# Kernel tuning notes

Hardware: AMD Instinct MI355X
Metric: run time of the kernel (lower is better)

The kernel has to match this reference:

```python
import jax, jax.numpy as jnp
import numpy as np

N = 50000
E = 800000
IN_DIM = 128
F_NUM = 64
OUT_DIM = 16


def gcn_norm(edge_index, edge_weight, num_nodes):
    # add self loops with fill value 1.0 (improved=False), then symmetric norm
    e = edge_index.shape[1]
    w = jnp.ones((e,), jnp.float32) if edge_weight is None else edge_weight
    loop = jnp.arange(num_nodes, dtype=edge_index.dtype)
    row = jnp.concatenate([edge_index[0], loop])
    col = jnp.concatenate([edge_index[1], loop])
    w = jnp.concatenate([w, jnp.ones((num_nodes,), jnp.float32)])
    deg = jax.ops.segment_sum(w, col, num_segments=num_nodes)
    dis = jnp.where(deg > 0, jax.lax.rsqrt(jnp.where(deg > 0, deg, 1.0)), 0.0)
    norm = dis[row] * w * dis[col]
    return row, col, norm


def dgconv(x, edge_index, edge_weight, num_nodes):
    row, col, norm = gcn_norm(edge_index, edge_weight, num_nodes)
    # gather -> scale -> scatter-add
    msg = norm[:, None] * x[row]          # [E+N, F]
    return jax.ops.segment_sum(msg, col, num_segments=num_nodes)


def setup_inputs() -> dict:
    key = jax.random.key(0)
    ks = jax.random.split(key, 12)
    x = jax.random.normal(ks[0], (N, IN_DIM), jnp.float32)
    edge_index = jax.random.randint(ks[1], (2, E), 0, N, jnp.int64 if jax.config.jax_enable_x64 else jnp.int32)
    edge_in = jax.random.randint(ks[2], (2, E), 0, N, edge_index.dtype)
    edge_out = jax.random.randint(ks[3], (2, E), 0, N, edge_index.dtype)
    in_w = jax.random.uniform(ks[4], (E,), jnp.float32)
    out_w = jax.random.uniform(ks[5], (E,), jnp.float32)
    lin1_w = jax.random.normal(ks[6], (F_NUM, IN_DIM), jnp.float32) / np.sqrt(IN_DIM)
    lin2_w = jax.random.normal(ks[7], (F_NUM, 3 * F_NUM), jnp.float32) / np.sqrt(3 * F_NUM)
    bias1 = jnp.zeros((1, F_NUM), jnp.float32)
    bias2 = jnp.zeros((1, F_NUM), jnp.float32)
    conv_w = jax.random.normal(ks[8], (OUT_DIM, 3 * F_NUM), jnp.float32) / np.sqrt(3 * F_NUM)
    conv_b = jnp.zeros((OUT_DIM,), jnp.float32)
    return {"x": x, "edge_index": edge_index, "edge_in": edge_in, "edge_out": edge_out,
            "in_w": in_w, "out_w": out_w, "lin1_w": lin1_w, "lin2_w": lin2_w,
            "bias1": bias1, "bias2": bias2, "conv_w": conv_w, "conv_b": conv_b}


def reference(x, edge_index, edge_in, edge_out, in_w, out_w,
              lin1_w, lin2_w, bias1, bias2, conv_w, conv_b):
    n = x.shape[0]
    h = x @ lin1_w.T                                          # [N, F]
    h1 = dgconv(h, edge_index, None, n) + bias1
    h2 = dgconv(h, edge_in, in_w, n) + bias1
    h3 = dgconv(h, edge_out, out_w, n) + bias1
    h = jax.nn.relu(jnp.concatenate([h1, h2, h3], axis=-1))   # [N, 3F]
    h = h @ lin2_w.T                                          # [N, F]
    h1 = dgconv(h, edge_index, None, n) + bias2
    h2 = dgconv(h, edge_in, in_w, n) + bias2
    h3 = dgconv(h, edge_out, out_w, n) + bias2
    h = jax.nn.relu(jnp.concatenate([h1, h2, h3], axis=-1))   # [N, 3F]
    # Conv1d(kernel_size=1) == pointwise linear over channels
    logits = h @ conv_w.T + conv_b                            # [N, out_dim]
    return jax.nn.log_softmax(logits, axis=1)
```

## Files before the change

kernel.cpp:

```cpp
#include <hip/hip_runtime.h>
#include <hip/hip_fp16.h>
#include <math.h>

#define FDIM 64
#define CATDIM 192
#define CH 2048
#define MAXNB 1024
#define SCTILE 2048


__global__ __launch_bounds__(256) void k_chist(const int* __restrict__ ei0,
                                               const int* __restrict__ ei1,
                                               const int* __restrict__ ei2,
                                               int* __restrict__ bhT,
                                               int NB, int nchunks, int E) {
    __shared__ int hist[MAXNB];
    const int c = blockIdx.x, g = blockIdx.y, tid = threadIdx.x;
    const int* dest = (g == 0 ? ei0 : g == 1 ? ei1 : ei2) + E;
    const size_t L = (size_t)NB * nchunks;

    for (int i = tid; i < NB; i += 256) hist[i] = 0;
    __syncthreads();

    const int lo = c * CH, hi = min(E, lo + CH);
    for (int i = lo + tid; i < hi; i += 256) atomicAdd(&hist[dest[i] >> 6], 1);
    __syncthreads();

    for (int i = tid; i < NB; i += 256)
        bhT[g * L + (size_t)c * NB + i] = hist[i];
}


__global__ __launch_bounds__(256) void k_tr(const int* __restrict__ in,
                                            int* __restrict__ out,
                                            int rows, int cols) {
    __shared__ int tile[32][33];
    const int g = blockIdx.z;
    const int c0 = blockIdx.x * 32;
    const int r0 = blockIdx.y * 32;
    const int tx = threadIdx.x & 31, ty0 = threadIdx.x >> 5;
    const size_t L = (size_t)rows * cols;
    const int* pin = in + (size_t)g * L;
    int* pout = out + (size_t)g * L;

    for (int dy = 0; dy < 32; dy += 8) {
        int r = r0 + ty0 + dy, c = c0 + tx;
        tile[ty0 + dy][tx] = (r < rows && c < cols) ? pin[(size_t)r * cols + c] : 0;
    }
    __syncthreads();
    for (int dy = 0; dy < 32; dy += 8) {
        int c = c0 + ty0 + dy, r = r0 + tx;
        if (c < cols && r < rows) pout[(size_t)c * rows + r] = tile[tx][ty0 + dy];
    }
}


__global__ __launch_bounds__(256) void k_scan_a(const int* __restrict__ bh,
                                                int* __restrict__ bsum,
                                                int L, int nblkS) {
    __shared__ int s[256];
    const int b = blockIdx.x, g = blockIdx.y, tid = threadIdx.x;
    const int* data = bh + (size_t)g * L;
    const int base = b * SCTILE + tid * 8;
    int v = 0;
#pragma unroll
    for (int j = 0; j < 8; ++j) {
        int idx = base + j;
        if (idx < L) v += data[idx];
    }
    s[tid] = v;
    __syncthreads();
    for (int d = 128; d > 0; d >>= 1) {
        if (tid < d) s[tid] += s[tid + d];
        __syncthreads();
    }
    if (tid == 0) bsum[g * nblkS + b] = s[0];
}

__global__ __launch_bounds__(256) void k_scan_b(int* __restrict__ bsum, int nblkS) {
    __shared__ int s[256];
    const int g = blockIdx.x, tid = threadIdx.x;
    int v = (tid < nblkS) ? bsum[g * nblkS + tid] : 0;
    s[tid] = v;
    __syncthreads();
    for (int d = 1; d < 256; d <<= 1) {
        int t = (tid >= d) ? s[tid - d] : 0;
        __syncthreads();
        s[tid] += t;
        __syncthreads();
    }
    if (tid < nblkS) bsum[g * nblkS + tid] = s[tid] - v;
}

__global__ __launch_bounds__(256) void k_scan_c(int* __restrict__ bh,
                                                const int* __restrict__ bsum,
                                                int L, int nblkS) {
    __shared__ int s[256];
    const int b = blockIdx.x, g = blockIdx.y, tid = threadIdx.x;
    int* data = bh + (size_t)g * L;
    const int base = b * SCTILE + tid * 8;

    int e[8];
    int tot = 0;
#pragma unroll
    for (int j = 0; j < 8; ++j) {
        e[j] = (base + j < L) ? data[base + j] : 0;
        tot += e[j];
    }
    s[tid] = tot;
    __syncthreads();
    for (int d = 1; d < 256; d <<= 1) {
        int t = (tid >= d) ? s[tid - d] : 0;
        __syncthreads();
        s[tid] += t;
        __syncthreads();
    }
    int run = bsum[g * nblkS + b] + s[tid] - tot;
#pragma unroll
    for (int j = 0; j < 8; ++j) {
        if (base + j < L) {
            int v = e[j];
            data[base + j] = run;
            run += v;
        }
    }
}


__global__ void k_bbase(const int* __restrict__ bh, int* __restrict__ bbase,
                        int NB, int nchunks, int E) {
    int i = blockIdx.x * blockDim.x + threadIdx.x;
    if (i >= 3 * NB) return;
    int g = i / NB, b = i - g * NB;
    bbase[g * (NB + 1) + b] = bh[((size_t)g * NB + b) * nchunks];
    if (b == 0) bbase[g * (NB + 1) + NB] = E;
}


__global__ __launch_bounds__(256) void k_cfill(const int* __restrict__ ei0,
                                               const int* __restrict__ ei1,
                                               const int* __restrict__ ei2,
                                               const float* __restrict__ w1,
                                               const float* __restrict__ w2,
                                               const int* __restrict__ bhT2,
                                               int2* __restrict__ barr,
                                               int NB, int nchunks, int E) {
    __shared__ int cur[MAXNB];
    const int c = blockIdx.x, g = blockIdx.y, tid = threadIdx.x;
    const int* e = (g == 0 ? ei0 : g == 1 ? ei1 : ei2);
    const float* w = (g == 1 ? w1 : w2);
    const int* srcp = e;
    const int* dest = e + E;
    int2* bout = barr + (size_t)g * E;
    const size_t L = (size_t)NB * nchunks;

    for (int i = tid; i < NB; i += 256)
        cur[i] = bhT2[g * L + (size_t)c * NB + i];
    __syncthreads();

    const int lo = c * CH, hi = min(E, lo + CH);
    for (int i = lo + tid; i < hi; i += 256) {
        int d = dest[i];
        int slot = atomicAdd(&cur[d >> 6], 1);
        float wv = (g == 0) ? 0.f : w[i];
        bout[slot] = make_int2(srcp[i] | ((d & 63) << 16), __float_as_int(wv));
    }
}


__global__ __launch_bounds__(256) void k_deg(const int2* __restrict__ barr,
                                             const int* __restrict__ bbase,
                                             int* __restrict__ rowptr,
                                             float* __restrict__ dis,
                                             int N, int E, int NB) {
    __shared__ int hist[64];
    __shared__ float wsum[64];
    __shared__ int sc[64];

    const int b = blockIdx.x, g = blockIdx.y, tid = threadIdx.x;
    const int2* bin = barr + (size_t)g * E;
    const int beg = bbase[g * (NB + 1) + b];
    const int end = bbase[g * (NB + 1) + b + 1];

    if (tid < 64) { hist[tid] = 0; wsum[tid] = 1.0f; }
    __syncthreads();

    for (int t = beg + tid; t < end; t += 256) {
        int2 p = bin[t];
        int dl = (p.x >> 16) & 63;
        atomicAdd(&hist[dl], 1);
        if (g) atomicAdd(&wsum[dl], __int_as_float(p.y));
    }
    __syncthreads();

    if (tid < 64) sc[tid] = hist[tid];
    __syncthreads();
    for (int d = 1; d < 64; d <<= 1) {
        int t = 0;
        if (tid < 64 && tid >= d) t = sc[tid - d];
        __syncthreads();
        if (tid < 64) sc[tid] += t;
        __syncthreads();
    }
    if (tid < 64) {
        int node = b * 64 + tid;
        if (node < N) {
            rowptr[g * (N + 1) + node] = beg + (sc[tid] - hist[tid]);
            float s = g ? wsum[tid] : (1.0f + (float)hist[tid]);
            dis[g * N + node] = rsqrtf(s);
        }
    }
    if (b == NB - 1 && tid == 0) rowptr[g * (N + 1) + N] = end;
}


__global__ __launch_bounds__(256) void k_place(const int2* __restrict__ barr,
                                               const int* __restrict__ bbase,
                                               const int* __restrict__ rowptr,
                                               const float* __restrict__ dis,
                                               unsigned* __restrict__ csr,
                                               int N, int E, int NB) {
    __shared__ int cur[64];
    const int b = blockIdx.x, g = blockIdx.y, tid = threadIdx.x;
    const int2* bin = barr + (size_t)g * E;
    const int beg = bbase[g * (NB + 1) + b];
    const int end = bbase[g * (NB + 1) + b + 1];

    if (tid < 64) {
        int node = b * 64 + tid;
        cur[tid] = (node < N) ? rowptr[g * (N + 1) + node] - beg : 0;
    }
    __syncthreads();

    for (int t = beg + tid; t < end; t += 256) {
        int2 p = bin[t];
        int dl = (p.x >> 16) & 63;
        int pos = atomicAdd(&cur[dl], 1);
        int src = p.x & 0xFFFF;
        float wv = g ? __int_as_float(p.y) : 1.0f;
        float v = wv * dis[g * N + src];
        unsigned short wb = __half_as_ushort(__float2half(v));
        csr[(size_t)g * E + beg + pos] = (unsigned)src | ((unsigned)wb << 16);
    }
}


template <typename T> __device__ inline float4 load4f(const T* p);
template <> __device__ inline float4 load4f<float>(const float* p) {
    return *reinterpret_cast<const float4*>(p);
}
template <> __device__ inline float4 load4f<__half>(const __half* p) {
    __half2 a = *reinterpret_cast<const __half2*>(p);
    __half2 b = *reinterpret_cast<const __half2*>(p + 2);
    float2 fa = __half22float2(a), fb = __half22float2(b);
    return make_float4(fa.x, fa.y, fb.x, fb.y);
}

template <int K, typename TA>
__global__ __launch_bounds__(256) void k_gemm(const TA* __restrict__ A,
                                              const float* __restrict__ W,
                                              __half* __restrict__ out, int n) {
    __shared__ float wt[K * 65];
    __shared__ float xs[64 * 36];

    const int tid = threadIdx.x;
    const int n0 = blockIdx.x * 64;

    for (int idx = tid; idx < FDIM * K; idx += 256) {
        int fr = idx / K;
        int kr = idx - fr * K;
        wt[kr * 65 + fr] = W[idx];
    }

    const int f = tid & 63;
    const int q = tid >> 6;
    float acc[16];
#pragma unroll
    for (int j = 0; j < 16; ++j) acc[j] = 0.f;

    for (int kc = 0; kc < K; kc += 32) {
        __syncthreads();
#pragma unroll
        for (int u = tid; u < 512; u += 256) {
            int node = u >> 3;
            int k4 = u & 7;
            int gn = n0 + node;
            float4 a = make_float4(0.f, 0.f, 0.f, 0.f);
            if (gn < n) a = load4f(&A[(size_t)gn * K + kc + k4 * 4]);
            *reinterpret_cast<float4*>(&xs[node * 36 + k4 * 4]) = a;
        }
        __syncthreads();

#pragma unroll
        for (int kk = 0; kk < 32; kk += 4) {
            float w0 = wt[(kc + kk + 0) * 65 + f];
            float w1 = wt[(kc + kk + 1) * 65 + f];
            float w2 = wt[(kc + kk + 2) * 65 + f];
            float w3 = wt[(kc + kk + 3) * 65 + f];
#pragma unroll
            for (int jj = 0; jj < 16; ++jj) {
                int j = jj * 4 + q;
                float4 av = *reinterpret_cast<const float4*>(&xs[j * 36 + kk]);
                acc[jj] = fmaf(av.x, w0, fmaf(av.y, w1, fmaf(av.z, w2, fmaf(av.w, w3, acc[jj]))));
            }
        }
    }

#pragma unroll
    for (int jj = 0; jj < 16; ++jj) {
        int node = n0 + jj * 4 + q;
        if (node < n) out[(size_t)node * FDIM + f] = __float2half(acc[jj]);
    }
}


__global__ __launch_bounds__(256) void k_gather(const __half* __restrict__ h,
                                                const float* __restrict__ dis,
                                                const int* __restrict__ rowptr,
                                                const unsigned* __restrict__ csr,
                                                const float* __restrict__ bias,
                                                __half* __restrict__ cat,
                                                int N, int E) {
    int i = blockIdx.x * 4 + (threadIdx.x >> 6);
    if (i >= N) return;
    const int lane = threadIdx.x & 63;

    const float hv = __half2float(h[(size_t)i * FDIM + lane]);
    const float b = bias[lane];

#pragma unroll
    for (int g = 0; g < 3; ++g) {
        const int* rp = rowptr + g * (N + 1);
        const unsigned* cg = csr + (size_t)g * E;
        const int beg = __builtin_amdgcn_readfirstlane(rp[i]);
        const int end = __builtin_amdgcn_readfirstlane(rp[i + 1]);
        float dg = dis[g * N + i];

        float acc0 = 0.f, acc1 = 0.f, acc2 = 0.f, acc3 = 0.f;
        float acc4 = 0.f, acc5 = 0.f, acc6 = 0.f, acc7 = 0.f;
        int j = beg;
        for (; j + 8 <= end; j += 8) {
            unsigned u0 = cg[j + 0];
            unsigned u1 = cg[j + 1];
            unsigned u2 = cg[j + 2];
            unsigned u3 = cg[j + 3];
            unsigned u4 = cg[j + 4];
            unsigned u5 = cg[j + 5];
            unsigned u6 = cg[j + 6];
            unsigned u7 = cg[j + 7];
            float a0 = __half2float(h[(size_t)(u0 & 0xFFFFu) * FDIM + lane]);
            float a1 = __half2float(h[(size_t)(u1 & 0xFFFFu) * FDIM + lane]);
            float a2 = __half2float(h[(size_t)(u2 & 0xFFFFu) * FDIM + lane]);
            float a3 = __half2float(h[(size_t)(u3 & 0xFFFFu) * FDIM + lane]);
            float a4 = __half2float(h[(size_t)(u4 & 0xFFFFu) * FDIM + lane]);
            float a5 = __half2float(h[(size_t)(u5 & 0xFFFFu) * FDIM + lane]);
            float a6 = __half2float(h[(size_t)(u6 & 0xFFFFu) * FDIM + lane]);
            float a7 = __half2float(h[(size_t)(u7 & 0xFFFFu) * FDIM + lane]);
            acc0 = fmaf(__half2float(__ushort_as_half((unsigned short)(u0 >> 16))), a0, acc0);
            acc1 = fmaf(__half2float(__ushort_as_half((unsigned short)(u1 >> 16))), a1, acc1);
            acc2 = fmaf(__half2float(__ushort_as_half((unsigned short)(u2 >> 16))), a2, acc2);
            acc3 = fmaf(__half2float(__ushort_as_half((unsigned short)(u3 >> 16))), a3, acc3);
            acc4 = fmaf(__half2float(__ushort_as_half((unsigned short)(u4 >> 16))), a4, acc4);
            acc5 = fmaf(__half2float(__ushort_as_half((unsigned short)(u5 >> 16))), a5, acc5);
            acc6 = fmaf(__half2float(__ushort_as_half((unsigned short)(u6 >> 16))), a6, acc6);
            acc7 = fmaf(__half2float(__ushort_as_half((unsigned short)(u7 >> 16))), a7, acc7);
        }
        if (j + 4 <= end) {
            unsigned u0 = cg[j + 0];
            unsigned u1 = cg[j + 1];
            unsigned u2 = cg[j + 2];
            unsigned u3 = cg[j + 3];
            float a0 = __half2float(h[(size_t)(u0 & 0xFFFFu) * FDIM + lane]);
            float a1 = __half2float(h[(size_t)(u1 & 0xFFFFu) * FDIM + lane]);
            float a2 = __half2float(h[(size_t)(u2 & 0xFFFFu) * FDIM + lane]);
            float a3 = __half2float(h[(size_t)(u3 & 0xFFFFu) * FDIM + lane]);
            acc0 = fmaf(__half2float(__ushort_as_half((unsigned short)(u0 >> 16))), a0, acc0);
            acc1 = fmaf(__half2float(__ushort_as_half((unsigned short)(u1 >> 16))), a1, acc1);
            acc2 = fmaf(__half2float(__ushort_as_half((unsigned short)(u2 >> 16))), a2, acc2);
            acc3 = fmaf(__half2float(__ushort_as_half((unsigned short)(u3 >> 16))), a3, acc3);
            j += 4;
        }
        for (; j < end; ++j) {
            unsigned u0 = cg[j];
            float a0 = __half2float(h[(size_t)(u0 & 0xFFFFu) * FDIM + lane]);
            acc0 = fmaf(__half2float(__ushort_as_half((unsigned short)(u0 >> 16))), a0, acc0);
        }
        float outv = dg * (((acc0 + acc1) + (acc2 + acc3)) + ((acc4 + acc5) + (acc6 + acc7)))
                   + dg * dg * hv + b;
        cat[(size_t)i * CATDIM + g * FDIM + lane] = __float2half(outv > 0.f ? outv : 0.f);
    }
}


__global__ __launch_bounds__(256) void k_final(const __half* __restrict__ cat,
                                               const float* __restrict__ convw,
                                               const float* __restrict__ convb,
                                               float* __restrict__ out, int n) {
    __shared__ float wl[16 * 196];
    __shared__ float bl[16];
    const int tid = threadIdx.x;
    for (int t = tid; t < 16 * 192; t += 256) {
        int o = t / 192;
        int k = t - o * 192;
        wl[o * 196 + k] = convw[t];
    }
    if (tid < 16) bl[tid] = convb[tid];
    __syncthreads();

    const int o = tid & 15;
    const int node = blockIdx.x * 16 + (tid >> 4);
    const int nc = node < n ? node : n - 1;

    const float4* xr4 = reinterpret_cast<const float4*>(cat + (size_t)nc * CATDIM);
    const float* wr = &wl[o * 196];
    float acc = bl[o];
#pragma unroll
    for (int k8 = 0; k8 < CATDIM / 8; ++k8) {
        float4 raw = xr4[k8];
        const __half2* hp = reinterpret_cast<const __half2*>(&raw);
        float2 f0 = __half22float2(hp[0]);
        float2 f1 = __half22float2(hp[1]);
        float2 f2 = __half22float2(hp[2]);
        float2 f3 = __half22float2(hp[3]);
        const float* w8 = wr + k8 * 8;
        acc += f0.x * w8[0] + f0.y * w8[1] + f1.x * w8[2] + f1.y * w8[3] +
               f2.x * w8[4] + f2.y * w8[5] + f3.x * w8[6] + f3.y * w8[7];
    }

    float m = acc;
    m = fmaxf(m, __shfl_xor(m, 1));
    m = fmaxf(m, __shfl_xor(m, 2));
    m = fmaxf(m, __shfl_xor(m, 4));
    m = fmaxf(m, __shfl_xor(m, 8));
    float s = __expf(acc - m);
    s += __shfl_xor(s, 1);
    s += __shfl_xor(s, 2);
    s += __shfl_xor(s, 4);
    s += __shfl_xor(s, 8);
    if (node < n) out[(size_t)node * 16 + o] = acc - m - logf(s);
}


extern "C" void kernel_launch(void* const* d_in, const int* in_sizes, int n_in,
                              void* d_out, int out_size, void* d_ws, size_t ws_size,
                              hipStream_t stream) {
    const float* x      = (const float*)d_in[0];
    const int*   ei     = (const int*)d_in[1];
    const int*   e_in   = (const int*)d_in[2];
    const int*   e_out  = (const int*)d_in[3];
    const float* in_w   = (const float*)d_in[4];
    const float* out_w  = (const float*)d_in[5];
    const float* lin1_w = (const float*)d_in[6];
    const float* lin2_w = (const float*)d_in[7];
    const float* bias1  = (const float*)d_in[8];
    const float* bias2  = (const float*)d_in[9];
    const float* conv_w = (const float*)d_in[10];
    const float* conv_b = (const float*)d_in[11];
    float* out = (float*)d_out;

    const int N = in_sizes[0] / 128;
    const int E = in_sizes[1] / 2;
    const int NB = (N + 63) >> 6;
    const int nchunks = (E + CH - 1) / CH;
    const int L = NB * nchunks;
    const int nblkS = (L + SCTILE - 1) / SCTILE;

    float* ws = (float*)d_ws;
    size_t o = 0;
    float* dis    = ws + o;            o += (size_t)3 * N;
    int*   rowptr = (int*)(ws + o);    o += ((size_t)3 * (N + 1) + 1) & ~1ull;
    int*   bbase  = (int*)(ws + o);    o += ((size_t)3 * (NB + 1) + 1) & ~1ull;
    int*   bsum   = (int*)(ws + o);    o += ((size_t)3 * nblkS + 1) & ~1ull;
    int*   bh     = (int*)(ws + o);    o += ((size_t)3 * L + 3) & ~3ull;
    int*   bhT    = (int*)(ws + o);    o += ((size_t)3 * L + 3) & ~3ull;
    __half* h     = (__half*)(ws + o); o += (size_t)N * (FDIM / 2);
    o = (o + 3) & ~3ull;
    unsigned* csr = (unsigned*)(ws + o); o += (size_t)3 * E;
    o = (o + 3) & ~3ull;
    __half* cat   = (__half*)(ws + o); o += (size_t)N * (CATDIM / 2);
    int2*  barr   = (int2*)cat;

    const int B = 256;

    hipLaunchKernelGGL(k_chist, dim3(nchunks, 3), dim3(B), 0, stream, ei, e_in, e_out, bhT, NB, nchunks, E);
    hipLaunchKernelGGL(k_tr, dim3((NB + 31) / 32, (nchunks + 31) / 32, 3), dim3(B), 0, stream,
                       bhT, bh, nchunks, NB);
    hipLaunchKernelGGL(k_scan_a, dim3(nblkS, 3), dim3(B), 0, stream, bh, bsum, L, nblkS);
    hipLaunchKernelGGL(k_scan_b, dim3(3), dim3(B), 0, stream, bsum, nblkS);
    hipLaunchKernelGGL(k_scan_c, dim3(nblkS, 3), dim3(B), 0, stream, bh, bsum, L, nblkS);
    hipLaunchKernelGGL(k_bbase, dim3((3 * NB + B - 1) / B), dim3(B), 0, stream, bh, bbase, NB, nchunks, E);
    hipLaunchKernelGGL(k_tr, dim3((nchunks + 31) / 32, (NB + 31) / 32, 3), dim3(B), 0, stream,
                       bh, bhT, NB, nchunks);
    hipLaunchKernelGGL(k_cfill, dim3(nchunks, 3), dim3(B), 0, stream,
                       ei, e_in, e_out, in_w, out_w, bhT, barr, NB, nchunks, E);
    hipLaunchKernelGGL(k_deg, dim3(NB, 3), dim3(B), 0, stream, barr, bbase, rowptr, dis, N, E, NB);
    hipLaunchKernelGGL(k_place, dim3(NB, 3), dim3(B), 0, stream, barr, bbase, rowptr, dis, csr, N, E, NB);

    hipLaunchKernelGGL((k_gemm<128, float>), dim3((N + 63) / 64), dim3(B), 0, stream, x, lin1_w, h, N);
    hipLaunchKernelGGL(k_gather, dim3((N + 3) / 4), dim3(B), 0, stream,
                       h, dis, rowptr, csr, bias1, cat, N, E);

    hipLaunchKernelGGL((k_gemm<192, __half>), dim3((N + 63) / 64), dim3(B), 0, stream, cat, lin2_w, h, N);
    hipLaunchKernelGGL(k_gather, dim3((N + 3) / 4), dim3(B), 0, stream,
                       h, dis, rowptr, csr, bias2, cat, N, E);

    hipLaunchKernelGGL(k_final, dim3((N + 15) / 16), dim3(B), 0, stream, cat, conv_w, conv_b, out, N);
}
```

Measured before the change: 413.7 us.

## Fuse final conv+log_softmax into gather, half2 gather lanes, chunk GEMM weights, fold bbase

Several changes land together. The final pointwise conv and log_softmax are fused into the second gather kernel, so the layer-two concat buffer is never written or read back. The gather now has each wave split into two halves that each process alternate edges with half2 feature loads, and the halves are combined with a cross-half shuffle. The GEMM stages weights in K-chunks to cut shared memory use and raise occupancy, and the bucket-base kernel is merged into the scan. In exchange, the fused gather loads the conv weights into LDS in every block and gains some branching in the per-edge index loads.

```diff
diff --git a/kernel.cpp b/kernel.cpp
--- a/kernel.cpp
+++ b/kernel.cpp
@@ -92,9 +92,12 @@
     if (tid < nblkS) bsum[g * nblkS + tid] = s[tid] - v;
 }
 
+
 __global__ __launch_bounds__(256) void k_scan_c(int* __restrict__ bh,
                                                 const int* __restrict__ bsum,
-                                                int L, int nblkS) {
+                                                int* __restrict__ bbase,
+                                                int L, int nblkS,
+                                                int NB, int nchunks, int E) {
     __shared__ int s[256];
     const int b = blockIdx.x, g = blockIdx.y, tid = threadIdx.x;
     int* data = bh + (size_t)g * L;
@@ -118,22 +121,15 @@
     int run = bsum[g * nblkS + b] + s[tid] - tot;
 #pragma unroll
     for (int j = 0; j < 8; ++j) {
-        if (base + j < L) {
+        int idx = base + j;
+        if (idx < L) {
             int v = e[j];
-            data[base + j] = run;
+            data[idx] = run;
+            if (idx % nchunks == 0) bbase[g * (NB + 1) + idx / nchunks] = run;
             run += v;
         }
     }
-}
-
-
-__global__ void k_bbase(const int* __restrict__ bh, int* __restrict__ bbase,
-                        int NB, int nchunks, int E) {
-    int i = blockIdx.x * blockDim.x + threadIdx.x;
-    if (i >= 3 * NB) return;
-    int g = i / NB, b = i - g * NB;
-    bbase[g * (NB + 1) + b] = bh[((size_t)g * NB + b) * nchunks];
-    if (b == 0) bbase[g * (NB + 1) + NB] = E;
+    if (b == 0 && tid == 0) bbase[g * (NB + 1) + NB] = E;
 }
 
 
@@ -256,21 +252,15 @@
     return make_float4(fa.x, fa.y, fb.x, fb.y);
 }
 
-template <int K, typename TA>
+template <int K, int KCH, typename TA>
 __global__ __launch_bounds__(256) void k_gemm(const TA* __restrict__ A,
                                               const float* __restrict__ W,
                                               __half* __restrict__ out, int n) {
-    __shared__ float wt[K * 65];
+    __shared__ float wt[KCH * 65];
     __shared__ float xs[64 * 36];
 
     const int tid = threadIdx.x;
     const int n0 = blockIdx.x * 64;
-
-    for (int idx = tid; idx < FDIM * K; idx += 256) {
-        int fr = idx / K;
-        int kr = idx - fr * K;
-        wt[kr * 65 + fr] = W[idx];
-    }
 
     const int f = tid & 63;
     const int q = tid >> 6;
@@ -280,6 +270,13 @@
 
     for (int kc = 0; kc < K; kc += 32) {
         __syncthreads();
+        if ((kc % KCH) == 0) {
+            for (int idx = tid; idx < FDIM * KCH; idx += 256) {
+                int fr = idx / KCH;
+                int kr = idx - fr * KCH;
+                wt[kr * 65 + fr] = W[fr * K + kc + kr];
+            }
+        }
 #pragma unroll
         for (int u = tid; u < 512; u += 256) {
             int node = u >> 3;
@@ -291,12 +288,13 @@
         }
         __syncthreads();
 
+        const int kb = kc % KCH;
 #pragma unroll
         for (int kk = 0; kk < 32; kk += 4) {
-            float w0 = wt[(kc + kk + 0) * 65 + f];
-            float w1 = wt[(kc + kk + 1) * 65 + f];
-            float w2 = wt[(kc + kk + 2) * 65 + f];
-            float w3 = wt[(kc + kk + 3) * 65 + f];
+            float w0 = wt[(kb + kk + 0) * 65 + f];
+            float w1 = wt[(kb + kk + 1) * 65 + f];
+            float w2 = wt[(kb + kk + 2) * 65 + f];
+            float w3 = wt[(kb + kk + 3) * 65 + f];
 #pragma unroll
             for (int jj = 0; jj < 16; ++jj) {
                 int j = jj * 4 + q;
@@ -314,19 +312,45 @@
 }
 
 
+template <int FUSE>
 __global__ __launch_bounds__(256) void k_gather(const __half* __restrict__ h,
                                                 const float* __restrict__ dis,
                                                 const int* __restrict__ rowptr,
                                                 const unsigned* __restrict__ csr,
                                                 const float* __restrict__ bias,
                                                 __half* __restrict__ cat,
+                                                const float* __restrict__ convw,
+                                                const float* __restrict__ convb,
+                                                float* __restrict__ outp,
                                                 int N, int E) {
-    int i = blockIdx.x * 4 + (threadIdx.x >> 6);
+    __shared__ float wl[FUSE ? 16 * 196 : 1];
+    __shared__ float bl[FUSE ? 16 : 1];
+    __shared__ float scratch[FUSE ? 4 : 1][FUSE ? 192 : 1];
+
+    const int tid = threadIdx.x;
+    if (FUSE) {
+        for (int t = tid; t < 16 * 192; t += 256) {
+            int o = t / 192;
+            int k = t - o * 192;
+            wl[o * 196 + k] = convw[t];
+        }
+        if (tid < 16) bl[tid] = convb[tid];
+        __syncthreads();
+    }
+
+    const int wv = tid >> 6;
+    const int lane = tid & 63;
+    const int fp = lane & 31;
+    const int ep = lane >> 5;
+    const int i = blockIdx.x * 4 + wv;
     if (i >= N) return;
-    const int lane = threadIdx.x & 63;
-
-    const float hv = __half2float(h[(size_t)i * FDIM + lane]);
-    const float b = bias[lane];
+
+    const __half2* h2 = reinterpret_cast<const __half2*>(h);
+    float2 hv = __half22float2(h2[(size_t)i * 32 + fp]);
+    const float b0 = bias[2 * fp];
+    const float b1 = bias[2 * fp + 1];
+
+    float res0[3], res1[3];
 
 #pragma unroll
     for (int g = 0; g < 3; ++g) {
@@ -334,110 +358,100 @@
         const unsigned* cg = csr + (size_t)g * E;
         const int beg = __builtin_amdgcn_readfirstlane(rp[i]);
         const int end = __builtin_amdgcn_readfirstlane(rp[i + 1]);
-        float dg = dis[g * N + i];
-
-        float acc0 = 0.f, acc1 = 0.f, acc2 = 0.f, acc3 = 0.f;
-        float acc4 = 0.f, acc5 = 0.f, acc6 = 0.f, acc7 = 0.f;
+        const float dg = dis[g * N + i];
+
+        float ax0 = 0.f, ay0 = 0.f, ax1 = 0.f, ay1 = 0.f;
+        float ax2 = 0.f, ay2 = 0.f, ax3 = 0.f, ay3 = 0.f;
         int j = beg;
         for (; j + 8 <= end; j += 8) {
-            unsigned u0 = cg[j + 0];
-            unsigned u1 = cg[j + 1];
-            unsigned u2 = cg[j + 2];
-            unsigned u3 = cg[j + 3];
-            unsigned u4 = cg[j + 4];
-            unsigned u5 = cg[j + 5];
-            unsigned u6 = cg[j + 6];
-            unsigned u7 = cg[j + 7];
-            float a0 = __half2float(h[(size_t)(u0 & 0xFFFFu) * FDIM + lane]);
-            float a1 = __half2float(h[(size_t)(u1 & 0xFFFFu) * FDIM + lane]);
-            float a2 = __half2float(h[(size_t)(u2 & 0xFFFFu) * FDIM + lane]);
-            float a3 = __half2float(h[(size_t)(u3 & 0xFFFFu) * FDIM + lane]);
-            float a4 = __half2float(h[(size_t)(u4 & 0xFFFFu) * FDIM + lane]);
-            float a5 = __half2float(h[(size_t)(u5 & 0xFFFFu) * FDIM + lane]);
-            float a6 = __half2float(h[(size_t)(u6 & 0xFFFFu) * FDIM + lane]);
-            float a7 = __half2float(h[(size_t)(u7 & 0xFFFFu) * FDIM + lane]);
-            acc0 = fmaf(__half2float(__ushort_as_half((unsigned short)(u0 >> 16))), a0, acc0);
-            acc1 = fmaf(__half2float(__ushort_as_half((unsigned short)(u1 >> 16))), a1, acc1);
-            acc2 = fmaf(__half2float(__ushort_as_half((unsigned short)(u2 >> 16))), a2, acc2);
-            acc3 = fmaf(__half2float(__ushort_as_half((unsigned short)(u3 >> 16))), a3, acc3);
-            acc4 = fmaf(__half2float(__ushort_as_half((unsigned short)(u4 >> 16))), a4, acc4);
-            acc5 = fmaf(__half2float(__ushort_as_half((unsigned short)(u5 >> 16))), a5, acc5);
-            acc6 = fmaf(__half2float(__ushort_as_half((unsigned short)(u6 >> 16))), a6, acc6);
-            acc7 = fmaf(__half2float(__ushort_as_half((unsigned short)(u7 >> 16))), a7, acc7);
+            unsigned u0 = ep ? cg[j + 1] : cg[j + 0];
+            unsigned u1 = ep ? cg[j + 3] : cg[j + 2];
+            unsigned u2 = ep ? cg[j + 5] : cg[j + 4];
+            unsigned u3 = ep ? cg[j + 7] : cg[j + 6];
+            float2 A0 = __half22float2(h2[(size_t)(u0 & 0xFFFFu) * 32 + fp]);
+            float2 A1 = __half22float2(h2[(size_t)(u1 & 0xFFFFu) * 32 + fp]);
+            float2 A2 = __half22float2(h2[(size_t)(u2 & 0xFFFFu) * 32 + fp]);
+            float2 A3 = __half22float2(h2[(size_t)(u3 & 0xFFFFu) * 32 + fp]);
+            float w0 = __half2float(__ushort_as_half((unsigned short)(u0 >> 16)));
+            float w1 = __half2float(__ushort_as_half((unsigned short)(u1 >> 16)));
+            float w2 = __half2float(__ushort_as_half((unsigned short)(u2 >> 16)));
+            float w3 = __half2float(__ushort_as_half((unsigned short)(u3 >> 16)));
+            ax0 = fmaf(w0, A0.x, ax0); ay0 = fmaf(w0, A0.y, ay0);
+            ax1 = fmaf(w1, A1.x, ax1); ay1 = fmaf(w1, A1.y, ay1);
+            ax2 = fmaf(w2, A2.x, ax2); ay2 = fmaf(w2, A2.y, ay2);
+            ax3 = fmaf(w3, A3.x, ax3); ay3 = fmaf(w3, A3.y, ay3);
         }
         if (j + 4 <= end) {
-            unsigned u0 = cg[j + 0];
-            unsigned u1 = cg[j + 1];
-            unsigned u2 = cg[j + 2];
-            unsigned u3 = cg[j + 3];
-            float a0 = __half2float(h[(size_t)(u0 & 0xFFFFu) * FDIM + lane]);
-            float a1 = __half2float(h[(size_t)(u1 & 0xFFFFu) * FDIM + lane]);
-            float a2 = __half2float(h[(size_t)(u2 & 0xFFFFu) * FDIM + lane]);
-            float a3 = __half2float(h[(size_t)(u3 & 0xFFFFu) * FDIM + lane]);
-            acc0 = fmaf(__half2float(__ushort_as_half((unsigned short)(u0 >> 16))), a0, acc0);
-            acc1 = fmaf(__half2float(__ushort_as_half((unsigned short)(u1 >> 16))), a1, acc1);
-            acc2 = fmaf(__half2float(__ushort_as_half((unsigned short)(u2 >> 16))), a2, acc2);
-            acc3 = fmaf(__half2float(__ushort_as_half((unsigned short)(u3 >> 16))), a3, acc3);
+            unsigned u0 = ep ? cg[j + 1] : cg[j + 0];
+            unsigned u1 = ep ? cg[j + 3] : cg[j + 2];
+            float2 A0 = __half22float2(h2[(size_t)(u0 & 0xFFFFu) * 32 + fp]);
+            float2 A1 = __half22float2(h2[(size_t)(u1 & 0xFFFFu) * 32 + fp]);
+            float w0 = __half2float(__ushort_as_half((unsigned short)(u0 >> 16)));
+            float w1 = __half2float(__ushort_as_half((unsigned short)(u1 >> 16)));
+            ax0 = fmaf(w0, A0.x, ax0); ay0 = fmaf(w0, A0.y, ay0);
+            ax1 = fmaf(w1, A1.x, ax1); ay1 = fmaf(w1, A1.y, ay1);
             j += 4;
         }
-        for (; j < end; ++j) {
-            unsigned u0 = cg[j];
-            float a0 = __half2float(h[(size_t)(u0 & 0xFFFFu) * FDIM + lane]);
-            acc0 = fmaf(__half2float(__ushort_as_half((unsigned short)(u0 >> 16))), a0, acc0);
-        }
-        float outv = dg * (((acc0 + acc1) + (acc2 + acc3)) + ((acc4 + acc5) + (acc6 + acc7)))
-                   + dg * dg * hv + b;
-        cat[(size_t)i * CATDIM + g * FDIM + lane] = __float2half(outv > 0.f ? outv : 0.f);
-    }
-}
-
-
-__global__ __launch_bounds__(256) void k_final(const __half* __restrict__ cat,
-                                               const float* __restrict__ convw,
-                                               const float* __restrict__ convb,
-                                               float* __restrict__ out, int n) {
-    __shared__ float wl[16 * 196];
-    __shared__ float bl[16];
-    const int tid = threadIdx.x;
-    for (int t = tid; t < 16 * 192; t += 256) {
-        int o = t / 192;
-        int k = t - o * 192;
-        wl[o * 196 + k] = convw[t];
-    }
-    if (tid < 16) bl[tid] = convb[tid];
-    __syncthreads();
-
-    const int o = tid & 15;
-    const int node = blockIdx.x * 16 + (tid >> 4);
-    const int nc = node < n ? node : n - 1;
-
-    const float4* xr4 = reinterpret_cast<const float4*>(cat + (size_t)nc * CATDIM);
-    const float* wr = &wl[o * 196];
-    float acc = bl[o];
-#pragma unroll
-    for (int k8 = 0; k8 < CATDIM / 8; ++k8) {
-        float4 raw = xr4[k8];
-        const __half2* hp = reinterpret_cast<const __half2*>(&raw);
-        float2 f0 = __half22float2(hp[0]);
-        float2 f1 = __half22float2(hp[1]);
-        float2 f2 = __half22float2(hp[2]);
-        float2 f3 = __half22float2(hp[3]);
-        const float* w8 = wr + k8 * 8;
-        acc += f0.x * w8[0] + f0.y * w8[1] + f1.x * w8[2] + f1.y * w8[3] +
-               f2.x * w8[4] + f2.y * w8[5] + f3.x * w8[6] + f3.y * w8[7];
-    }
-
-    float m = acc;
-    m = fmaxf(m, __shfl_xor(m, 1));
-    m = fmaxf(m, __shfl_xor(m, 2));
-    m = fmaxf(m, __shfl_xor(m, 4));
-    m = fmaxf(m, __shfl_xor(m, 8));
-    float s = __expf(acc - m);
-    s += __shfl_xor(s, 1);
-    s += __shfl_xor(s, 2);
-    s += __shfl_xor(s, 4);
-    s += __shfl_xor(s, 8);
-    if (node < n) out[(size_t)node * 16 + o] = acc - m - logf(s);
+        while (j < end) {
+            unsigned ulo = cg[j];
+            unsigned uhi = (j + 1 < end) ? cg[j + 1] : 0u;
+            unsigned u0 = ep ? uhi : ulo;
+            float2 A0 = __half22float2(h2[(size_t)(u0 & 0xFFFFu) * 32 + fp]);
+            float w0 = __half2float(__ushort_as_half((unsigned short)(u0 >> 16)));
+            ax0 = fmaf(w0, A0.x, ax0); ay0 = fmaf(w0, A0.y, ay0);
+            j += 2;
+        }
+
+        float sx = (ax0 + ax1) + (ax2 + ax3);
+        float sy = (ay0 + ay1) + (ay2 + ay3);
+        sx += __shfl_xor(sx, 32);
+        sy += __shfl_xor(sy, 32);
+        float r0 = fmaf(dg, sx, dg * dg * hv.x) + b0;
+        float r1 = fmaf(dg, sy, dg * dg * hv.y) + b1;
+        res0[g] = r0 > 0.f ? r0 : 0.f;
+        res1[g] = r1 > 0.f ? r1 : 0.f;
+    }
+
+    if (!FUSE) {
+        if (ep == 0) {
+            __half2* c2 = reinterpret_cast<__half2*>(cat);
+#pragma unroll
+            for (int g = 0; g < 3; ++g)
+                c2[(size_t)i * 96 + g * 32 + fp] = __floats2half2_rn(res0[g], res1[g]);
+        }
+    } else {
+        if (ep == 0) {
+            float2* sp = reinterpret_cast<float2*>(&scratch[wv][0]);
+#pragma unroll
+            for (int g = 0; g < 3; ++g)
+                sp[g * 32 + fp] = make_float2(res0[g], res1[g]);
+        }
+        const int o = lane & 15;
+        const int seg = lane >> 4;
+        const float* xr = &scratch[wv][seg * 48];
+        const float* wr = &wl[o * 196 + seg * 48];
+        float acc = 0.f;
+#pragma unroll
+        for (int k4 = 0; k4 < 12; ++k4) {
+            float4 xv = *reinterpret_cast<const float4*>(xr + k4 * 4);
+            float4 wv4 = *reinterpret_cast<const float4*>(wr + k4 * 4);
+            acc += xv.x * wv4.x + xv.y * wv4.y + xv.z * wv4.z + xv.w * wv4.w;
+        }
+        acc += __shfl_xor(acc, 16);
+        acc += __shfl_xor(acc, 32);
+        acc += bl[o];
+        float m = acc;
+        m = fmaxf(m, __shfl_xor(m, 1));
+        m = fmaxf(m, __shfl_xor(m, 2));
+        m = fmaxf(m, __shfl_xor(m, 4));
+        m = fmaxf(m, __shfl_xor(m, 8));
+        float s = __expf(acc - m);
+        s += __shfl_xor(s, 1);
+        s += __shfl_xor(s, 2);
+        s += __shfl_xor(s, 4);
+        s += __shfl_xor(s, 8);
+        if (lane < 16) outp[(size_t)i * 16 + o] = acc - m - logf(s);
+    }
 }
 
 
@@ -487,8 +501,7 @@
                        bhT, bh, nchunks, NB);
     hipLaunchKernelGGL(k_scan_a, dim3(nblkS, 3), dim3(B), 0, stream, bh, bsum, L, nblkS);
     hipLaunchKernelGGL(k_scan_b, dim3(3), dim3(B), 0, stream, bsum, nblkS);
-    hipLaunchKernelGGL(k_scan_c, dim3(nblkS, 3), dim3(B), 0, stream, bh, bsum, L, nblkS);
-    hipLaunchKernelGGL(k_bbase, dim3((3 * NB + B - 1) / B), dim3(B), 0, stream, bh, bbase, NB, nchunks, E);
+    hipLaunchKernelGGL(k_scan_c, dim3(nblkS, 3), dim3(B), 0, stream, bh, bsum, bbase, L, nblkS, NB, nchunks, E);
     hipLaunchKernelGGL(k_tr, dim3((nchunks + 31) / 32, (NB + 31) / 32, 3), dim3(B), 0, stream,
                        bh, bhT, NB, nchunks);
     hipLaunchKernelGGL(k_cfill, dim3(nchunks, 3), dim3(B), 0, stream,
@@ -496,13 +509,13 @@
     hipLaunchKernelGGL(k_deg, dim3(NB, 3), dim3(B), 0, stream, barr, bbase, rowptr, dis, N, E, NB);
     hipLaunchKernelGGL(k_place, dim3(NB, 3), dim3(B), 0, stream, barr, bbase, rowptr, dis, csr, N, E, NB);
 
-    hipLaunchKernelGGL((k_gemm<128, float>), dim3((N + 63) / 64), dim3(B), 0, stream, x, lin1_w, h, N);
-    hipLaunchKernelGGL(k_gather, dim3((N + 3) / 4), dim3(B), 0, stream,
-                       h, dis, rowptr, csr, bias1, cat, N, E);
-
-    hipLaunchKernelGGL((k_gemm<192, __half>), dim3((N + 63) / 64), dim3(B), 0, stream, cat, lin2_w, h, N);
-    hipLaunchKernelGGL(k_gather, dim3((N + 3) / 4), dim3(B), 0, stream,
-                       h, dis, rowptr, csr, bias2, cat, N, E);
-
-    hipLaunchKernelGGL(k_final, dim3((N + 15) / 16), dim3(B), 0, stream, cat, conv_w, conv_b, out, N);
-}
+    hipLaunchKernelGGL((k_gemm<128, 64, float>), dim3((N + 63) / 64), dim3(B), 0, stream, x, lin1_w, h, N);
+    hipLaunchKernelGGL((k_gather<0>), dim3((N + 3) / 4), dim3(B), 0, stream,
+                       h, dis, rowptr, csr, bias1, cat,
+                       (const float*)nullptr, (const float*)nullptr, (float*)nullptr, N, E);
+
+    hipLaunchKernelGGL((k_gemm<192, 96, __half>), dim3((N + 63) / 64), dim3(B), 0, stream, cat, lin2_w, h, N);
+    hipLaunchKernelGGL((k_gather<1>), dim3((N + 3) / 4), dim3(B), 0, stream,
+                       h, dis, rowptr, csr, bias2, (__half*)nullptr,
+                       conv_w, conv_b, out, N, E);
+}
```

New measurement: 420.9 us. About the same (+1.7%).
